# Performance work log

Measured on AMD Instinct MI355X. Metric: run time of the kernel, lower is better.

The kernel has to match this reference:

```python
import jax, jax.numpy as jnp
import numpy as np

N_NODES = 100000
N_EDGES = 1600000
N_GRAPHS = 64
FEAT = 64
EMB = 64
HID = 64
VOCAB = 32


def setup_inputs() -> dict:
    key = jax.random.key(0)
    ks = jax.random.split(key, 20)
    w = lambda k, sh: (jax.random.normal(k, sh, jnp.float32) * 0.05)
    x = jax.random.normal(ks[0], (N_NODES, FEAT), jnp.float32)
    edge_index = jax.random.randint(ks[1], (2, N_EDGES), 0, N_NODES, dtype=jnp.int32).astype(jnp.int64)
    batch = jnp.sort(jax.random.randint(ks[2], (N_NODES,), 0, N_GRAPHS, dtype=jnp.int32)).astype(jnp.int64)
    return {
        'x': x, 'edge_index': edge_index, 'batch': batch,
        # RGCN layer 1 (single relation): relation weight, root weight, bias
        'W1': w(ks[3], (FEAT, EMB)), 'root1': w(ks[4], (FEAT, EMB)), 'b1': w(ks[5], (EMB,)),
        # RGCN layer 2
        'W2': w(ks[6], (EMB, HID)), 'root2': w(ks[7], (EMB, HID)), 'b2': w(ks[8], (HID,)),
        # init_h / init_c linear heads
        'Wh': w(ks[9], (HID, HID)), 'bh': w(ks[10], (HID,)),
        'Wc': w(ks[11], (HID, HID)), 'bc': w(ks[12], (HID,)),
        # output layer
        'Wo': w(ks[13], (HID, VOCAB)), 'bo': w(ks[14], (VOCAB,)),
    }


def _rgcn(x, edge_index, W, root, b):
    # PyG RGCNConv with num_relations=1, aggr='mean':
    # out[i] = mean_{j in N(i)} (x[j] @ W) + x[i] @ root + b
    src, dst = edge_index[0], edge_index[1]
    msg = x[src] @ W                                    # [E, out] gather + small GEMM
    agg = jax.ops.segment_sum(msg, dst, num_segments=x.shape[0])
    cnt = jax.ops.segment_sum(jnp.ones((edge_index.shape[1],), x.dtype), dst, num_segments=x.shape[0])
    agg = agg / jnp.maximum(cnt, 1.0)[:, None]
    return agg + x @ root + b


def reference(x, edge_index, batch, W1, root1, b1, W2, root2, b2, Wh, bh, Wc, bc, Wo, bo):
    h = jax.nn.relu(_rgcn(x, edge_index, W1, root1, b1))
    h = jax.nn.relu(_rgcn(h, edge_index, W2, root2, b2))
    # global_mean_pool over graph-assignment vector `batch`
    summ = jax.ops.segment_sum(h, batch, num_segments=N_GRAPHS)
    cnt = jax.ops.segment_sum(jnp.ones((h.shape[0],), h.dtype), batch, num_segments=N_GRAPHS)
    pooled = summ / jnp.maximum(cnt, 1.0)[:, None]      # [G, HID]
    hidden = pooled @ Wh + bh
    cell = pooled @ Wc + bc
    logits = jax.nn.log_softmax(hidden @ Wo + bo, axis=1)
    return (logits, hidden, cell)
```

## Files before the change

kernel.cpp:

```cpp
#include <hip/hip_runtime.h>
#include <hip/hip_bf16.h>


typedef __attribute__((ext_vector_type(8))) short short8;
typedef __attribute__((ext_vector_type(4))) float f32x4;

#define RB 9
#define MAXBINS 256
#define CAP 12288
#define BCAP 14336
#define CHUNK 8192

__device__ inline float bf2f(unsigned short h) {
    return __uint_as_float(((unsigned int)h) << 16);
}
__device__ inline float bflo(unsigned int u) { return __uint_as_float(u << 16); }
__device__ inline float bfhi(unsigned int u) { return __uint_as_float(u & 0xffff0000u); }
__device__ inline unsigned short f2bf(float f) {
    unsigned int u = __float_as_uint(f);
    u = (u + 0x7fffu + ((u >> 16) & 1u)) >> 16;
    return (unsigned short)u;
}

__global__ __launch_bounds__(256) void bin_prep(const int* __restrict__ src,
                                                const int* __restrict__ dst,
                                                unsigned int* __restrict__ coarse,
                                                int* __restrict__ gcur,
                                                int E, int BINS, int nbBin,
                                                const float* __restrict__ W1,
                                                const float* __restrict__ R1,
                                                const float* __restrict__ W2,
                                                const float* __restrict__ R2,
                                                unsigned short* __restrict__ bt) {
    __shared__ int cnt[MAXBINS];
    __shared__ int incl[MAXBINS];
    __shared__ int bstart[MAXBINS];
    __shared__ int bcur[MAXBINS];
    __shared__ int gbase[MAXBINS];
    __shared__ unsigned int stage[CHUNK];
    __shared__ unsigned char binOf[CHUNK];

    const int tid = threadIdx.x;
    if (blockIdx.x >= nbBin) {
        const int layer = blockIdx.x - nbBin;
        const float* W = layer ? W2 : W1;
        const float* R = layer ? R2 : R1;
        unsigned short* o = bt + (size_t)layer * 8192;
        for (int idx = tid; idx < 8192; idx += 256) {
            const int n = idx >> 6, k = idx & 63;
            const float v = (n < 64) ? W[k * 64 + n] : R[k * 64 + (n - 64)];
            o[idx] = f2bf(v);
        }
        return;
    }

    const int chunk0 = blockIdx.x * CHUNK;
    int myS[32], myD[32];
#pragma unroll
    for (int k = 0; k < 32; ++k) {
        const int idx = chunk0 + k * 256 + tid;
        if (idx < E) { myS[k] = src[idx]; myD[k] = dst[idx]; }
        else myD[k] = -1;
    }
    cnt[tid] = 0;
    __syncthreads();
#pragma unroll
    for (int k = 0; k < 32; ++k)
        if (myD[k] >= 0) atomicAdd(&cnt[myD[k] >> RB], 1);
    __syncthreads();
    incl[tid] = cnt[tid];
    __syncthreads();
    for (int off = 1; off < 256; off <<= 1) {
        int t = (tid >= off) ? incl[tid - off] : 0;
        __syncthreads();
        incl[tid] += t;
        __syncthreads();
    }
    bstart[tid] = incl[tid] - cnt[tid];
    bcur[tid] = incl[tid] - cnt[tid];
    __syncthreads();
#pragma unroll
    for (int k = 0; k < 32; ++k) {
        if (myD[k] >= 0) {
            const int b = myD[k] >> RB;
            const int pos = atomicAdd(&bcur[b], 1);
            stage[pos] = (unsigned int)myS[k] | ((unsigned int)(myD[k] & ((1 << RB) - 1)) << 17);
            binOf[pos] = (unsigned char)b;
        }
    }
    __syncthreads();
    if (tid < BINS && cnt[tid] > 0)
        gbase[tid] = tid * CAP + atomicAdd(&gcur[tid], cnt[tid]);
    __syncthreads();
    int total = E - chunk0;
    if (total > CHUNK) total = CHUNK;
    for (int idx = tid; idx < total; idx += 256) {
        const int b = binOf[idx];
        coarse[gbase[b] + (idx - bstart[b])] = stage[idx];
    }
}

__global__ __launch_bounds__(256) void fin_gemm1(const unsigned int* __restrict__ coarse,
                                                 const int* __restrict__ gcur,
                                                 int* __restrict__ bucket,
                                                 int* __restrict__ pstart,
                                                 int* __restrict__ degarr,
                                                 int N, int BINS,
                                                 const float* __restrict__ x,
                                                 const unsigned short* __restrict__ bt,
                                                 const float* __restrict__ bias,
                                                 unsigned short* __restrict__ xw,
                                                 unsigned short* __restrict__ xrb) {
    __shared__ int ncnt[512];
    __shared__ int pexcl[512];
    __shared__ int ncur[512];
    __shared__ int s2[256];
    __shared__ int ptot;

    const int tid = threadIdx.x;
    if (blockIdx.x < (unsigned)BINS) {
        const int b = blockIdx.x;
        const int cb = gcur[b];
        const int base = b * BCAP;
        const unsigned int* reg = coarse + (size_t)b * CAP;
        const int node0 = b << RB;
        int nloc = N - node0;
        if (nloc > 512) nloc = 512;

        ncnt[tid] = 0; ncnt[tid + 256] = 0;
        __syncthreads();
        for (int idx = tid; idx < cb; idx += 256)
            atomicAdd(&ncnt[reg[idx] >> 17], 1);
        __syncthreads();
        const int p0 = (ncnt[2 * tid] + 15) & ~15;
        const int p1 = (ncnt[2 * tid + 1] + 15) & ~15;
        s2[tid] = p0 + p1;
        __syncthreads();
        for (int off = 1; off < 256; off <<= 1) {
            int t = (tid >= off) ? s2[tid - off] : 0;
            __syncthreads();
            s2[tid] += t;
            __syncthreads();
        }
        const int pairExcl = s2[tid] - (p0 + p1);
        pexcl[2 * tid] = pairExcl;
        pexcl[2 * tid + 1] = pairExcl + p0;
        ncur[2 * tid] = pairExcl;
        ncur[2 * tid + 1] = pairExcl + p0;
        if (tid == 255) ptot = s2[255];
        __syncthreads();
        const int total = ptot;
        for (int i = tid; i < nloc; i += 256) {
            pstart[node0 + i] = base + pexcl[i];
            degarr[node0 + i] = ncnt[i];
        }
        for (int idx = tid; idx < total; idx += 256) bucket[base + idx] = N;
        __syncthreads();
        for (int idx = tid; idx < cb; idx += 256) {
            const unsigned int e = reg[idx];
            const int p = atomicAdd(&ncur[e >> 17], 1);
            bucket[base + p] = (int)(e & 0x1FFFFu);
        }
        return;
    }

    const int gb = blockIdx.x - BINS;
    if (gb == 0 && tid < 32)
        *(unsigned int*)&xw[(size_t)N * 64 + tid * 2] = 0u;

    const int lane = tid & 63;
    const int q = lane >> 4;
    const int mm = lane & 15;

    short8 bfrag[8][2];
#pragma unroll
    for (int t = 0; t < 8; ++t)
#pragma unroll
        for (int c = 0; c < 2; ++c)
            bfrag[t][c] = *(const short8*)&bt[(size_t)(t * 16 + mm) * 64 + c * 32 + q * 8];
    float bv[4];
#pragma unroll
    for (int tt = 0; tt < 4; ++tt) bv[tt] = bias[tt * 16 + mm];

    const int wid = tid >> 6;
    const int gw = gb * 4 + wid;
    const int nw = 1024 * 4;
    const int ntiles = N >> 4;

    for (int tile = gw; tile < ntiles; tile += nw) {
        const int row0 = tile << 4;
        const float* ap = &x[(size_t)(row0 + mm) * 64 + q * 8];
        const float4 f0 = *(const float4*)ap;
        const float4 f1 = *(const float4*)(ap + 4);
        const float4 f2 = *(const float4*)(ap + 32);
        const float4 f3 = *(const float4*)(ap + 36);
        short8 a0, a1;
        a0[0] = (short)f2bf(f0.x); a0[1] = (short)f2bf(f0.y);
        a0[2] = (short)f2bf(f0.z); a0[3] = (short)f2bf(f0.w);
        a0[4] = (short)f2bf(f1.x); a0[5] = (short)f2bf(f1.y);
        a0[6] = (short)f2bf(f1.z); a0[7] = (short)f2bf(f1.w);
        a1[0] = (short)f2bf(f2.x); a1[1] = (short)f2bf(f2.y);
        a1[2] = (short)f2bf(f2.z); a1[3] = (short)f2bf(f2.w);
        a1[4] = (short)f2bf(f3.x); a1[5] = (short)f2bf(f3.y);
        a1[6] = (short)f2bf(f3.z); a1[7] = (short)f2bf(f3.w);
        f32x4 acc[8];
#pragma unroll
        for (int t = 0; t < 8; ++t) {
            acc[t] = (f32x4){0.f, 0.f, 0.f, 0.f};
            acc[t] = __builtin_amdgcn_mfma_f32_16x16x32_bf16(a0, bfrag[t][0], acc[t], 0, 0, 0);
            acc[t] = __builtin_amdgcn_mfma_f32_16x16x32_bf16(a1, bfrag[t][1], acc[t], 0, 0, 0);
        }
#pragma unroll
        for (int t = 0; t < 4; ++t) {
#pragma unroll
            for (int r = 0; r < 4; ++r) {
                const float v = acc[t][r];
                const float vn = __shfl_down(v, 1);
                if (!(mm & 1)) {
                    const unsigned int u = (unsigned int)f2bf(v) | ((unsigned int)f2bf(vn) << 16);
                    *(unsigned int*)&xw[(size_t)(row0 + q * 4 + r) * 64 + t * 16 + mm] = u;
                }
            }
        }
#pragma unroll
        for (int t = 4; t < 8; ++t) {
#pragma unroll
            for (int r = 0; r < 4; ++r) {
                const float v = acc[t][r] + bv[t - 4];
                const float vn = __shfl_down(v, 1);
                if (!(mm & 1)) {
                    const unsigned int u = (unsigned int)f2bf(v) | ((unsigned int)f2bf(vn) << 16);
                    *(unsigned int*)&xrb[(size_t)(row0 + q * 4 + r) * 64 + (t - 4) * 16 + mm] = u;
                }
            }
        }
    }
}

__global__ __launch_bounds__(256) void gemm_xwr(const unsigned short* __restrict__ xin,
                                                const unsigned short* __restrict__ bt,
                                                const float* __restrict__ bias,
                                                unsigned short* __restrict__ xw,
                                                unsigned short* __restrict__ xrb,
                                                int M) {
    if (blockIdx.x == 0 && threadIdx.x < 32)
        *(unsigned int*)&xw[(size_t)M * 64 + threadIdx.x * 2] = 0u;

    const int lane = threadIdx.x & 63;
    const int q = lane >> 4;
    const int mm = lane & 15;

    short8 bfrag[8][2];
#pragma unroll
    for (int t = 0; t < 8; ++t)
#pragma unroll
        for (int c = 0; c < 2; ++c)
            bfrag[t][c] = *(const short8*)&bt[(size_t)(t * 16 + mm) * 64 + c * 32 + q * 8];
    float bv[4];
#pragma unroll
    for (int tt = 0; tt < 4; ++tt) bv[tt] = bias[tt * 16 + mm];

    const int wid = threadIdx.x >> 6;
    const int gw = blockIdx.x * 4 + wid;
    const int nw = gridDim.x * 4;
    const int ntiles = M >> 4;

    for (int tile = gw; tile < ntiles; tile += nw) {
        const int row0 = tile << 4;
        const short8 a0 = *(const short8*)&xin[(size_t)(row0 + mm) * 64 + q * 8];
        const short8 a1 = *(const short8*)&xin[(size_t)(row0 + mm) * 64 + 32 + q * 8];
        f32x4 acc[8];
#pragma unroll
        for (int t = 0; t < 8; ++t) {
            acc[t] = (f32x4){0.f, 0.f, 0.f, 0.f};
            acc[t] = __builtin_amdgcn_mfma_f32_16x16x32_bf16(a0, bfrag[t][0], acc[t], 0, 0, 0);
            acc[t] = __builtin_amdgcn_mfma_f32_16x16x32_bf16(a1, bfrag[t][1], acc[t], 0, 0, 0);
        }
#pragma unroll
        for (int t = 0; t < 4; ++t) {
#pragma unroll
            for (int r = 0; r < 4; ++r) {
                const float v = acc[t][r];
                const float vn = __shfl_down(v, 1);
                if (!(mm & 1)) {
                    const unsigned int u = (unsigned int)f2bf(v) | ((unsigned int)f2bf(vn) << 16);
                    *(unsigned int*)&xw[(size_t)(row0 + q * 4 + r) * 64 + t * 16 + mm] = u;
                }
            }
        }
#pragma unroll
        for (int t = 4; t < 8; ++t) {
#pragma unroll
            for (int r = 0; r < 4; ++r) {
                const float v = acc[t][r] + bv[t - 4];
                const float vn = __shfl_down(v, 1);
                if (!(mm & 1)) {
                    const unsigned int u = (unsigned int)f2bf(v) | ((unsigned int)f2bf(vn) << 16);
                    *(unsigned int*)&xrb[(size_t)(row0 + q * 4 + r) * 64 + (t - 4) * 16 + mm] = u;
                }
            }
        }
    }
}

__device__ inline void agg_steps(const unsigned short* __restrict__ xw, int s, int t0, int t1,
                                 int half, int fl,
                                 float& l0, float& l1, float& l2, float& l3,
                                 float& h0, float& h1, float& h2, float& h3) {
    for (int t = t0; t < t1; t += 16) {
        unsigned int u[8];
#pragma unroll
        for (int p = 0; p < 8; ++p) {
            const int rr = __shfl(s, t + 2 * p + half);
            u[p] = *(const unsigned int*)&xw[(size_t)rr * 64 + fl * 2];
        }
        l0 += bflo(u[0]); h0 += bfhi(u[0]);
        l1 += bflo(u[1]); h1 += bfhi(u[1]);
        l2 += bflo(u[2]); h2 += bfhi(u[2]);
        l3 += bflo(u[3]); h3 += bfhi(u[3]);
        l0 += bflo(u[4]); h0 += bfhi(u[4]);
        l1 += bflo(u[5]); h1 += bfhi(u[5]);
        l2 += bflo(u[6]); h2 += bfhi(u[6]);
        l3 += bflo(u[7]); h3 += bfhi(u[7]);
    }
}

__global__ __launch_bounds__(256) void aggregate(const unsigned short* __restrict__ xw,
                                                 const unsigned short* __restrict__ xrb,
                                                 const int* __restrict__ pstart,
                                                 const int* __restrict__ degarr,
                                                 const int* __restrict__ bucket,
                                                 unsigned short* __restrict__ outb,
                                                 int N) {
    const int lane = threadIdx.x & 63;
    const int half = lane >> 5;
    const int fl = lane & 31;
    const int wid = threadIdx.x >> 6;
    const int gw = blockIdx.x * 4 + wid;
    const int nw = gridDim.x * 4;

    for (int i = gw; i < N; i += 2 * nw) {
        const int iB = i + nw;
        const int hasB = (iB < N);
        const int r0A = pstart[i];
        const int dgA = degarr[i];
        const int r0B = hasB ? pstart[iB] : r0A;
        const int dgB = hasB ? degarr[iB] : 0;
        const int pA = (dgA + 15) & ~15;
        const int pB = (dgB + 15) & ~15;

        float lA0 = 0.f, lA1 = 0.f, lA2 = 0.f, lA3 = 0.f;
        float hA0 = 0.f, hA1 = 0.f, hA2 = 0.f, hA3 = 0.f;
        float lB0 = 0.f, lB1 = 0.f, lB2 = 0.f, lB3 = 0.f;
        float hB0 = 0.f, hB1 = 0.f, hB2 = 0.f, hB3 = 0.f;

        if (pA <= 64 && pB <= 64) {
            const int sA = bucket[r0A + lane];
            const int sB = bucket[r0B + lane];
            const int pmax = pA > pB ? pA : pB;
            for (int t = 0; t < pmax; t += 16) {
                unsigned int uA[8], uB[8];
                const bool doA = t < pA, doB = t < pB;
                if (doA) {
#pragma unroll
                    for (int p = 0; p < 8; ++p) {
                        const int rr = __shfl(sA, t + 2 * p + half);
                        uA[p] = *(const unsigned int*)&xw[(size_t)rr * 64 + fl * 2];
                    }
                }
                if (doB) {
#pragma unroll
                    for (int p = 0; p < 8; ++p) {
                        const int rr = __shfl(sB, t + 2 * p + half);
                        uB[p] = *(const unsigned int*)&xw[(size_t)rr * 64 + fl * 2];
                    }
                }
                if (doA) {
                    lA0 += bflo(uA[0]); hA0 += bfhi(uA[0]);
                    lA1 += bflo(uA[1]); hA1 += bfhi(uA[1]);
                    lA2 += bflo(uA[2]); hA2 += bfhi(uA[2]);
                    lA3 += bflo(uA[3]); hA3 += bfhi(uA[3]);
                    lA0 += bflo(uA[4]); hA0 += bfhi(uA[4]);
                    lA1 += bflo(uA[5]); hA1 += bfhi(uA[5]);
                    lA2 += bflo(uA[6]); hA2 += bfhi(uA[6]);
                    lA3 += bflo(uA[7]); hA3 += bfhi(uA[7]);
                }
                if (doB) {
                    lB0 += bflo(uB[0]); hB0 += bfhi(uB[0]);
                    lB1 += bflo(uB[1]); hB1 += bfhi(uB[1]);
                    lB2 += bflo(uB[2]); hB2 += bfhi(uB[2]);
                    lB3 += bflo(uB[3]); hB3 += bfhi(uB[3]);
                    lB0 += bflo(uB[4]); hB0 += bfhi(uB[4]);
                    lB1 += bflo(uB[5]); hB1 += bfhi(uB[5]);
                    lB2 += bflo(uB[6]); hB2 += bfhi(uB[6]);
                    lB3 += bflo(uB[7]); hB3 += bfhi(uB[7]);
                }
            }
        } else {
            for (int base = 0; base < pA; base += 64) {
                const int rem = pA - base;
                const int s = (lane < rem) ? bucket[r0A + base + lane] : N;
                const int mmx = rem < 64 ? rem : 64;
                agg_steps(xw, s, 0, mmx, half, fl, lA0, lA1, lA2, lA3, hA0, hA1, hA2, hA3);
            }
            for (int base = 0; base < pB; base += 64) {
                const int rem = pB - base;
                const int s = (lane < rem) ? bucket[r0B + base + lane] : N;
                const int mmx = rem < 64 ? rem : 64;
                agg_steps(xw, s, 0, mmx, half, fl, lB0, lB1, lB2, lB3, hB0, hB1, hB2, hB3);
            }
        }

        float loA = (lA0 + lA1) + (lA2 + lA3);
        float hiA = (hA0 + hA1) + (hA2 + hA3);
        float loB = (lB0 + lB1) + (lB2 + lB3);
        float hiB = (hB0 + hB1) + (hB2 + hB3);
        loA += __shfl_xor(loA, 32); hiA += __shfl_xor(hiA, 32);
        loB += __shfl_xor(loB, 32); hiB += __shfl_xor(hiB, 32);

        const float invA = 1.0f / (float)(dgA > 0 ? dgA : 1);
        const float invB = 1.0f / (float)(dgB > 0 ? dgB : 1);
        const int row = (hasB && half) ? iB : i;
        const float mylo = half ? loB * invB : loA * invA;
        const float myhi = half ? hiB * invB : hiA * invA;
        const unsigned int ur = *(const unsigned int*)&xrb[(size_t)row * 64 + fl * 2];
        const float o0 = fmaxf(mylo + bflo(ur), 0.f);
        const float o1 = fmaxf(myhi + bfhi(ur), 0.f);
        if (hasB || half == 0) {
            const unsigned int u = (unsigned int)f2bf(o0) | ((unsigned int)f2bf(o1) << 16);
            *(unsigned int*)&outb[(size_t)row * 64 + fl * 2] = u;
        }
    }
}

__global__ __launch_bounds__(256) void pool_kernel(const unsigned short* __restrict__ h,
                                                   const int* __restrict__ batch,
                                                   float* __restrict__ pooled, int N) {
    __shared__ float red[16][64];
    __shared__ int bnds[2];
    const int gph = blockIdx.x;
    if (threadIdx.x < 2) {
        const int target = gph + threadIdx.x;
        int lo = 0, hi = N;
        while (lo < hi) {
            int mid = (lo + hi) >> 1;
            if (batch[mid] < target) lo = mid + 1; else hi = mid;
        }
        bnds[threadIdx.x] = lo;
    }
    __syncthreads();
    const int r0 = bnds[0], r1 = bnds[1];
    const int f = threadIdx.x & 15;
    const int r = threadIdx.x >> 4;
    float4 acc = {0.f, 0.f, 0.f, 0.f};
    for (int row = r0 + r; row < r1; row += 16) {
        const ushort4 v = *(const ushort4*)&h[(size_t)row * 64 + f * 4];
        acc.x += bf2f(v.x); acc.y += bf2f(v.y);
        acc.z += bf2f(v.z); acc.w += bf2f(v.w);
    }
    red[r][f * 4 + 0] = acc.x; red[r][f * 4 + 1] = acc.y;
    red[r][f * 4 + 2] = acc.z; red[r][f * 4 + 3] = acc.w;
    __syncthreads();
    if (threadIdx.x < 64) {
        float s = 0.f;
        for (int j = 0; j < 16; ++j) s += red[j][threadIdx.x];
        const int cnt = r1 - r0;
        const float invc = 1.0f / (float)(cnt > 0 ? cnt : 1);
        pooled[gph * 64 + threadIdx.x] = s * invc;
    }
}

__global__ __launch_bounds__(256) void head_kernel(const float* __restrict__ pooled,
                                                   const float* __restrict__ Wh,
                                                   const float* __restrict__ bh,
                                                   const float* __restrict__ Wc,
                                                   const float* __restrict__ bc,
                                                   const float* __restrict__ Wo,
                                                   const float* __restrict__ bo,
                                                   float* __restrict__ out) {
    __shared__ float pm[4096];
    __shared__ float hid[4096];
    __shared__ float lg[2048];
    const int t = threadIdx.x;

    for (int idx = t; idx < 4096; idx += 256) pm[idx] = pooled[idx];
    __syncthreads();

    for (int idx = t; idx < 4096; idx += 256) {
        int g = idx >> 6, o = idx & 63;
        float ah = bh[o], ac = bc[o];
        for (int k = 0; k < 64; ++k) {
            float p = pm[(g << 6) + k];
            ah += p * Wh[k * 64 + o];
            ac += p * Wc[k * 64 + o];
        }
        hid[idx] = ah;
        out[2048 + idx] = ah;
        out[6144 + idx] = ac;
    }
    __syncthreads();

    for (int idx = t; idx < 2048; idx += 256) {
        int g = idx >> 5, v = idx & 31;
        float a = bo[v];
        for (int k = 0; k < 64; ++k) a += hid[(g << 6) + k] * Wo[k * 32 + v];
        lg[idx] = a;
    }
    __syncthreads();

    if (t < 64) {
        float mx = -3.4e38f;
        for (int v = 0; v < 32; ++v) mx = fmaxf(mx, lg[(t << 5) + v]);
        float s = 0.f;
        for (int v = 0; v < 32; ++v) s += expf(lg[(t << 5) + v] - mx);
        float lse = mx + logf(s);
        for (int v = 0; v < 32; ++v) out[(t << 5) + v] = lg[(t << 5) + v] - lse;
    }
}

extern "C" void kernel_launch(void* const* d_in, const int* in_sizes, int n_in,
                              void* d_out, int out_size, void* d_ws, size_t ws_size,
                              hipStream_t stream) {
    const float* x = (const float*)d_in[0];
    const int* ei = (const int*)d_in[1];
    const int* batch = (const int*)d_in[2];
    const float* W1 = (const float*)d_in[3];
    const float* root1 = (const float*)d_in[4];
    const float* b1 = (const float*)d_in[5];
    const float* W2 = (const float*)d_in[6];
    const float* root2 = (const float*)d_in[7];
    const float* b2 = (const float*)d_in[8];
    const float* Wh = (const float*)d_in[9];
    const float* bh = (const float*)d_in[10];
    const float* Wc = (const float*)d_in[11];
    const float* bc = (const float*)d_in[12];
    const float* Wo = (const float*)d_in[13];
    const float* bo = (const float*)d_in[14];
    float* out = (float*)d_out;

    const int N = in_sizes[0] / 64;
    const int E = in_sizes[1] / 2;
    const int* srcp = ei;
    const int* dstp = ei + E;
    const int BINS = (N + (1 << RB) - 1) >> RB;

    char* ws = (char*)d_ws;
    size_t off = 0;
    auto alloc = [&](size_t bytes) -> void* {
        void* p = ws + off;
        off += (bytes + 255) & ~(size_t)255;
        return p;
    };
    int* pstart = (int*)alloc((size_t)N * 4);
    int* degarr = (int*)alloc((size_t)N * 4);
    int* bucket = (int*)alloc(((size_t)BINS * BCAP + 256) * 4);
    unsigned int* coarse = (unsigned int*)alloc((size_t)BINS * CAP * 4);
    unsigned short* h1 = (unsigned short*)alloc((size_t)N * 64 * 2);
    unsigned short* h2 = (unsigned short*)alloc((size_t)N * 64 * 2);
    unsigned short* xw = (unsigned short*)alloc((size_t)(N + 1) * 64 * 2);
    unsigned short* xrb = (unsigned short*)alloc((size_t)N * 64 * 2);
    unsigned short* bt = (unsigned short*)alloc(2 * 8192 * 2);
    float* pooled = (float*)alloc(4096 * 4);
    int* gcur = (int*)alloc(MAXBINS * 4);

    const int nbBin = (E + CHUNK - 1) / CHUNK;

    hipMemsetAsync(gcur, 0, MAXBINS * 4, stream);
    bin_prep<<<nbBin + 2, 256, 0, stream>>>(srcp, dstp, coarse, gcur, E, BINS, nbBin,
                                            W1, root1, W2, root2, bt);
    fin_gemm1<<<BINS + 1024, 256, 0, stream>>>(coarse, gcur, bucket, pstart, degarr, N, BINS,
                                               x, bt, b1, xw, xrb);
    aggregate<<<2048, 256, 0, stream>>>(xw, xrb, pstart, degarr, bucket, h1, N);
    gemm_xwr<<<1024, 256, 0, stream>>>(h1, bt + 8192, b2, xw, xrb, N);
    aggregate<<<2048, 256, 0, stream>>>(xw, xrb, pstart, degarr, bucket, h2, N);

    pool_kernel<<<64, 256, 0, stream>>>(h2, batch, pooled, N);
    head_kernel<<<1, 256, 0, stream>>>(pooled, Wh, bh, Wc, bc, Wo, bo, out);
}
```

Before: 301.9 us.

## Store projected messages in FP8 and gather 64-byte rows in aggregation

The per-node message features x@W are now written as packed FP8 (4 values per 32-bit word) rather than bf16, which halves the bytes each edge gather reads. The aggregate kernel is restructured so that each wave handles one node with 16 lanes per neighbour row and 4 neighbours per step, using hardware FP8-to-f32 unpacking. It then reduces across quarters with shuffles. The grid is doubled. FP8 quantisation of messages adds precision error, and the old two-node interleaving is removed.

Measured after the change: 282.2 us. 1.07x faster.

```diff
diff --git a/kernel.cpp b/kernel.cpp
--- a/kernel.cpp
+++ b/kernel.cpp
@@ -4,6 +4,7 @@
 
 typedef __attribute__((ext_vector_type(8))) short short8;
 typedef __attribute__((ext_vector_type(4))) float f32x4;
+typedef __attribute__((ext_vector_type(2))) float f32x2;
 
 #define RB 9
 #define MAXBINS 256
@@ -100,6 +101,22 @@
     }
 }
 
+__device__ inline void store_xw_fp8(unsigned char* __restrict__ xw8, int rowbase, int q,
+                                    int t, int mm, const f32x4& accT) {
+#pragma unroll
+    for (int r = 0; r < 4; ++r) {
+        const float v0 = accT[r];
+        const float v1 = __shfl_down(v0, 1);
+        const float v2 = __shfl_down(v0, 2);
+        const float v3 = __shfl_down(v0, 3);
+        if (!(mm & 3)) {
+            unsigned int u = (unsigned int)__builtin_amdgcn_cvt_pk_fp8_f32(v0, v1, 0, false);
+            u = (unsigned int)__builtin_amdgcn_cvt_pk_fp8_f32(v2, v3, (int)u, true);
+            *(unsigned int*)&xw8[(size_t)(rowbase + q * 4 + r) * 64 + t * 16 + mm] = u;
+        }
+    }
+}
+
 __global__ __launch_bounds__(256) void fin_gemm1(const unsigned int* __restrict__ coarse,
                                                  const int* __restrict__ gcur,
                                                  int* __restrict__ bucket,
@@ -109,7 +126,7 @@
                                                  const float* __restrict__ x,
                                                  const unsigned short* __restrict__ bt,
                                                  const float* __restrict__ bias,
-                                                 unsigned short* __restrict__ xw,
+                                                 unsigned char* __restrict__ xw8,
                                                  unsigned short* __restrict__ xrb) {
     __shared__ int ncnt[512];
     __shared__ int pexcl[512];
@@ -165,8 +182,8 @@
     }
 
     const int gb = blockIdx.x - BINS;
-    if (gb == 0 && tid < 32)
-        *(unsigned int*)&xw[(size_t)N * 64 + tid * 2] = 0u;
+    if (gb == 0 && tid < 16)
+        *(unsigned int*)&xw8[(size_t)N * 64 + tid * 4] = 0u;
 
     const int lane = tid & 63;
     const int q = lane >> 4;
@@ -211,17 +228,7 @@
             acc[t] = __builtin_amdgcn_mfma_f32_16x16x32_bf16(a1, bfrag[t][1], acc[t], 0, 0, 0);
         }
 #pragma unroll
-        for (int t = 0; t < 4; ++t) {
-#pragma unroll
-            for (int r = 0; r < 4; ++r) {
-                const float v = acc[t][r];
-                const float vn = __shfl_down(v, 1);
-                if (!(mm & 1)) {
-                    const unsigned int u = (unsigned int)f2bf(v) | ((unsigned int)f2bf(vn) << 16);
-                    *(unsigned int*)&xw[(size_t)(row0 + q * 4 + r) * 64 + t * 16 + mm] = u;
-                }
-            }
-        }
+        for (int t = 0; t < 4; ++t) store_xw_fp8(xw8, row0, q, t, mm, acc[t]);
 #pragma unroll
         for (int t = 4; t < 8; ++t) {
 #pragma unroll
@@ -240,11 +247,11 @@
 __global__ __launch_bounds__(256) void gemm_xwr(const unsigned short* __restrict__ xin,
                                                 const unsigned short* __restrict__ bt,
                                                 const float* __restrict__ bias,
-                                                unsigned short* __restrict__ xw,
+                                                unsigned char* __restrict__ xw8,
                                                 unsigned short* __restrict__ xrb,
                                                 int M) {
-    if (blockIdx.x == 0 && threadIdx.x < 32)
-        *(unsigned int*)&xw[(size_t)M * 64 + threadIdx.x * 2] = 0u;
+    if (blockIdx.x == 0 && threadIdx.x < 16)
+        *(unsigned int*)&xw8[(size_t)M * 64 + threadIdx.x * 4] = 0u;
 
     const int lane = threadIdx.x & 63;
     const int q = lane >> 4;
@@ -277,17 +284,7 @@
             acc[t] = __builtin_amdgcn_mfma_f32_16x16x32_bf16(a1, bfrag[t][1], acc[t], 0, 0, 0);
         }
 #pragma unroll
-        for (int t = 0; t < 4; ++t) {
-#pragma unroll
-            for (int r = 0; r < 4; ++r) {
-                const float v = acc[t][r];
-                const float vn = __shfl_down(v, 1);
-                if (!(mm & 1)) {
-                    const unsigned int u = (unsigned int)f2bf(v) | ((unsigned int)f2bf(vn) << 16);
-                    *(unsigned int*)&xw[(size_t)(row0 + q * 4 + r) * 64 + t * 16 + mm] = u;
-                }
-            }
-        }
+        for (int t = 0; t < 4; ++t) store_xw_fp8(xw8, row0, q, t, mm, acc[t]);
 #pragma unroll
         for (int t = 4; t < 8; ++t) {
 #pragma unroll
@@ -303,29 +300,7 @@
     }
 }
 
-__device__ inline void agg_steps(const unsigned short* __restrict__ xw, int s, int t0, int t1,
-                                 int half, int fl,
-                                 float& l0, float& l1, float& l2, float& l3,
-                                 float& h0, float& h1, float& h2, float& h3) {
-    for (int t = t0; t < t1; t += 16) {
-        unsigned int u[8];
-#pragma unroll
-        for (int p = 0; p < 8; ++p) {
-            const int rr = __shfl(s, t + 2 * p + half);
-            u[p] = *(const unsigned int*)&xw[(size_t)rr * 64 + fl * 2];
-        }
-        l0 += bflo(u[0]); h0 += bfhi(u[0]);
-        l1 += bflo(u[1]); h1 += bfhi(u[1]);
-        l2 += bflo(u[2]); h2 += bfhi(u[2]);
-        l3 += bflo(u[3]); h3 += bfhi(u[3]);
-        l0 += bflo(u[4]); h0 += bfhi(u[4]);
-        l1 += bflo(u[5]); h1 += bfhi(u[5]);
-        l2 += bflo(u[6]); h2 += bfhi(u[6]);
-        l3 += bflo(u[7]); h3 += bfhi(u[7]);
-    }
-}
-
-__global__ __launch_bounds__(256) void aggregate(const unsigned short* __restrict__ xw,
+__global__ __launch_bounds__(256) void aggregate(const unsigned char* __restrict__ xw8,
                                                  const unsigned short* __restrict__ xrb,
                                                  const int* __restrict__ pstart,
                                                  const int* __restrict__ degarr,
@@ -333,102 +308,52 @@
                                                  unsigned short* __restrict__ outb,
                                                  int N) {
     const int lane = threadIdx.x & 63;
-    const int half = lane >> 5;
-    const int fl = lane & 31;
+    const int quarter = lane >> 4;
+    const int fl = lane & 15;
     const int wid = threadIdx.x >> 6;
     const int gw = blockIdx.x * 4 + wid;
     const int nw = gridDim.x * 4;
 
-    for (int i = gw; i < N; i += 2 * nw) {
-        const int iB = i + nw;
-        const int hasB = (iB < N);
-        const int r0A = pstart[i];
-        const int dgA = degarr[i];
-        const int r0B = hasB ? pstart[iB] : r0A;
-        const int dgB = hasB ? degarr[iB] : 0;
-        const int pA = (dgA + 15) & ~15;
-        const int pB = (dgB + 15) & ~15;
-
-        float lA0 = 0.f, lA1 = 0.f, lA2 = 0.f, lA3 = 0.f;
-        float hA0 = 0.f, hA1 = 0.f, hA2 = 0.f, hA3 = 0.f;
-        float lB0 = 0.f, lB1 = 0.f, lB2 = 0.f, lB3 = 0.f;
-        float hB0 = 0.f, hB1 = 0.f, hB2 = 0.f, hB3 = 0.f;
-
-        if (pA <= 64 && pB <= 64) {
-            const int sA = bucket[r0A + lane];
-            const int sB = bucket[r0B + lane];
-            const int pmax = pA > pB ? pA : pB;
-            for (int t = 0; t < pmax; t += 16) {
-                unsigned int uA[8], uB[8];
-                const bool doA = t < pA, doB = t < pB;
-                if (doA) {
-#pragma unroll
-                    for (int p = 0; p < 8; ++p) {
-                        const int rr = __shfl(sA, t + 2 * p + half);
-                        uA[p] = *(const unsigned int*)&xw[(size_t)rr * 64 + fl * 2];
-                    }
+    for (int i = gw; i < N; i += nw) {
+        const int r0 = pstart[i];
+        const int dg = degarr[i];
+        const int pdeg = (dg + 15) & ~15;
+        float a0 = 0.f, a1 = 0.f, a2 = 0.f, a3 = 0.f;
+        for (int base = 0; base < pdeg; base += 64) {
+            const int rem = pdeg - base;
+            const int s = (lane < rem) ? bucket[r0 + base + lane] : N;
+            const int mm = rem < 64 ? rem : 64;
+            for (int t = 0; t < mm; t += 16) {
+                unsigned int u[4];
+#pragma unroll
+                for (int p = 0; p < 4; ++p) {
+                    const int rr = __shfl(s, t + 4 * p + quarter);
+                    u[p] = *(const unsigned int*)&xw8[(size_t)rr * 64 + fl * 4];
                 }
-                if (doB) {
-#pragma unroll
-                    for (int p = 0; p < 8; ++p) {
-                        const int rr = __shfl(sB, t + 2 * p + half);
-                        uB[p] = *(const unsigned int*)&xw[(size_t)rr * 64 + fl * 2];
-                    }
-                }
-                if (doA) {
-                    lA0 += bflo(uA[0]); hA0 += bfhi(uA[0]);
-                    lA1 += bflo(uA[1]); hA1 += bfhi(uA[1]);
-                    lA2 += bflo(uA[2]); hA2 += bfhi(uA[2]);
-                    lA3 += bflo(uA[3]); hA3 += bfhi(uA[3]);
-                    lA0 += bflo(uA[4]); hA0 += bfhi(uA[4]);
-                    lA1 += bflo(uA[5]); hA1 += bfhi(uA[5]);
-                    lA2 += bflo(uA[6]); hA2 += bfhi(uA[6]);
-                    lA3 += bflo(uA[7]); hA3 += bfhi(uA[7]);
-                }
-                if (doB) {
-                    lB0 += bflo(uB[0]); hB0 += bfhi(uB[0]);
-                    lB1 += bflo(uB[1]); hB1 += bfhi(uB[1]);
-                    lB2 += bflo(uB[2]); hB2 += bfhi(uB[2]);
-                    lB3 += bflo(uB[3]); hB3 += bfhi(uB[3]);
-                    lB0 += bflo(uB[4]); hB0 += bfhi(uB[4]);
-                    lB1 += bflo(uB[5]); hB1 += bfhi(uB[5]);
-                    lB2 += bflo(uB[6]); hB2 += bfhi(uB[6]);
-                    lB3 += bflo(uB[7]); hB3 += bfhi(uB[7]);
+#pragma unroll
+                for (int p = 0; p < 4; ++p) {
+                    const f32x2 lo = __builtin_amdgcn_cvt_pk_f32_fp8(u[p], false);
+                    const f32x2 hi = __builtin_amdgcn_cvt_pk_f32_fp8(u[p], true);
+                    a0 += lo.x; a1 += lo.y; a2 += hi.x; a3 += hi.y;
                 }
             }
-        } else {
-            for (int base = 0; base < pA; base += 64) {
-                const int rem = pA - base;
-                const int s = (lane < rem) ? bucket[r0A + base + lane] : N;
-                const int mmx = rem < 64 ? rem : 64;
-                agg_steps(xw, s, 0, mmx, half, fl, lA0, lA1, lA2, lA3, hA0, hA1, hA2, hA3);
-            }
-            for (int base = 0; base < pB; base += 64) {
-                const int rem = pB - base;
-                const int s = (lane < rem) ? bucket[r0B + base + lane] : N;
-                const int mmx = rem < 64 ? rem : 64;
-                agg_steps(xw, s, 0, mmx, half, fl, lB0, lB1, lB2, lB3, hB0, hB1, hB2, hB3);
-            }
-        }
-
-        float loA = (lA0 + lA1) + (lA2 + lA3);
-        float hiA = (hA0 + hA1) + (hA2 + hA3);
-        float loB = (lB0 + lB1) + (lB2 + lB3);
-        float hiB = (hB0 + hB1) + (hB2 + hB3);
-        loA += __shfl_xor(loA, 32); hiA += __shfl_xor(hiA, 32);
-        loB += __shfl_xor(loB, 32); hiB += __shfl_xor(hiB, 32);
-
-        const float invA = 1.0f / (float)(dgA > 0 ? dgA : 1);
-        const float invB = 1.0f / (float)(dgB > 0 ? dgB : 1);
-        const int row = (hasB && half) ? iB : i;
-        const float mylo = half ? loB * invB : loA * invA;
-        const float myhi = half ? hiB * invB : hiA * invA;
-        const unsigned int ur = *(const unsigned int*)&xrb[(size_t)row * 64 + fl * 2];
-        const float o0 = fmaxf(mylo + bflo(ur), 0.f);
-        const float o1 = fmaxf(myhi + bfhi(ur), 0.f);
-        if (hasB || half == 0) {
-            const unsigned int u = (unsigned int)f2bf(o0) | ((unsigned int)f2bf(o1) << 16);
-            *(unsigned int*)&outb[(size_t)row * 64 + fl * 2] = u;
+        }
+        a0 += __shfl_xor(a0, 16); a1 += __shfl_xor(a1, 16);
+        a2 += __shfl_xor(a2, 16); a3 += __shfl_xor(a3, 16);
+        a0 += __shfl_xor(a0, 32); a1 += __shfl_xor(a1, 32);
+        a2 += __shfl_xor(a2, 32); a3 += __shfl_xor(a3, 32);
+
+        const float inv = 1.0f / (float)(dg > 0 ? dg : 1);
+        if (quarter == 0) {
+            const uint2 ur = *(const uint2*)&xrb[(size_t)i * 64 + fl * 4];
+            const float o0 = fmaxf(a0 * inv + bflo(ur.x), 0.f);
+            const float o1 = fmaxf(a1 * inv + bfhi(ur.x), 0.f);
+            const float o2 = fmaxf(a2 * inv + bflo(ur.y), 0.f);
+            const float o3 = fmaxf(a3 * inv + bfhi(ur.y), 0.f);
+            uint2 w;
+            w.x = (unsigned int)f2bf(o0) | ((unsigned int)f2bf(o1) << 16);
+            w.y = (unsigned int)f2bf(o2) | ((unsigned int)f2bf(o3) << 16);
+            *(uint2*)&outb[(size_t)i * 64 + fl * 4] = w;
         }
     }
 }
@@ -557,7 +482,7 @@
     unsigned int* coarse = (unsigned int*)alloc((size_t)BINS * CAP * 4);
     unsigned short* h1 = (unsigned short*)alloc((size_t)N * 64 * 2);
     unsigned short* h2 = (unsigned short*)alloc((size_t)N * 64 * 2);
-    unsigned short* xw = (unsigned short*)alloc((size_t)(N + 1) * 64 * 2);
+    unsigned char* xw8 = (unsigned char*)alloc((size_t)(N + 1) * 64);
     unsigned short* xrb = (unsigned short*)alloc((size_t)N * 64 * 2);
     unsigned short* bt = (unsigned short*)alloc(2 * 8192 * 2);
     float* pooled = (float*)alloc(4096 * 4);
@@ -569,10 +494,10 @@
     bin_prep<<<nbBin + 2, 256, 0, stream>>>(srcp, dstp, coarse, gcur, E, BINS, nbBin,
                                             W1, root1, W2, root2, bt);
     fin_gemm1<<<BINS + 1024, 256, 0, stream>>>(coarse, gcur, bucket, pstart, degarr, N, BINS,
-                                               x, bt, b1, xw, xrb);
-    aggregate<<<2048, 256, 0, stream>>>(xw, xrb, pstart, degarr, bucket, h1, N);
-    gemm_xwr<<<1024, 256, 0, stream>>>(h1, bt + 8192, b2, xw, xrb, N);
-    aggregate<<<2048, 256, 0, stream>>>(xw, xrb, pstart, degarr, bucket, h2, N);
+                                               x, bt, b1, xw8, xrb);
+    aggregate<<<4096, 256, 0, stream>>>(xw8, xrb, pstart, degarr, bucket, h1, N);
+    gemm_xwr<<<1024, 256, 0, stream>>>(h1, bt + 8192, b2, xw8, xrb, N);
+    aggregate<<<4096, 256, 0, stream>>>(xw8, xrb, pstart, degarr, bucket, h2, N);
 
     pool_kernel<<<64, 256, 0, stream>>>(h2, batch, pooled, N);
     head_kernel<<<1, 256, 0, stream>>>(pooled, Wh, bh, Wc, bc, Wo, bo, out);
```
